# Optimization experiments

Measured on AMD Instinct MI355X. Metric: run time of the kernel, lower is better.

## Reference

```python
import jax, jax.numpy as jnp
import numpy as np

N, D, H, L = 100000, 128, 4, 2
C = D // H  # per-head channels
E = 1600000
NEG_SLOPE = 0.2
LN_EPS = 1e-5


def setup_inputs() -> dict:
    key = jax.random.key(0)
    ks = jax.random.split(key, 8)
    x = jax.random.normal(ks[0], (N, D), dtype=jnp.float32)
    edge_index = jax.random.randint(ks[1], (2, E), 0, N, dtype=jnp.int64)
    s = 1.0 / np.sqrt(D)
    Wl = jax.random.normal(ks[2], (L, D, D), dtype=jnp.float32) * s
    Wr = jax.random.normal(ks[3], (L, D, D), dtype=jnp.float32) * s
    att = jax.random.normal(ks[4], (L, H, C), dtype=jnp.float32) * (1.0 / np.sqrt(C))
    bias = jnp.zeros((L, D), dtype=jnp.float32)
    gamma = jnp.ones((L, D), dtype=jnp.float32)
    beta = jnp.zeros((L, D), dtype=jnp.float32)
    return {"x": x, "edge_index": edge_index, "Wl": Wl, "Wr": Wr,
            "att": att, "bias": bias, "gamma": gamma, "beta": beta}


def _gatv2_layer(h, src, dst, Wl, Wr, att, bias):
    # h: (N, D); src/dst: (E2,) with self-loops already appended
    xl = (h @ Wl).reshape(N, H, C)  # source-side transform
    xr = (h @ Wr).reshape(N, H, C)  # target-side transform
    e = jax.nn.leaky_relu(xl[src] + xr[dst], NEG_SLOPE)      # (E2, H, C)
    alpha = jnp.einsum('ehc,hc->eh', e, att)                 # (E2, H)
    # segment softmax over incoming edges of each destination node
    m = jax.ops.segment_max(alpha, dst, num_segments=N)      # (N, H)
    ea = jnp.exp(alpha - m[dst])
    s = jax.ops.segment_sum(ea, dst, num_segments=N)         # (N, H)
    a = ea / s[dst]                                          # (E2, H)
    out = jax.ops.segment_sum(a[:, :, None] * xl[src], dst, num_segments=N)
    return out.reshape(N, D) + bias


def _layer_norm(y, gamma, beta):
    mu = jnp.mean(y, axis=-1, keepdims=True)
    var = jnp.var(y, axis=-1, keepdims=True)
    return (y - mu) * jax.lax.rsqrt(var + LN_EPS) * gamma + beta


def reference(x, edge_index, Wl, Wr, att, bias, gamma, beta):
    # PyG GATv2Conv defaults: add_self_loops=True (eval mode: dropouts identity)
    loops = jnp.arange(N, dtype=edge_index.dtype)
    src = jnp.concatenate([edge_index[0], loops])
    dst = jnp.concatenate([edge_index[1], loops])
    h = x
    for l in range(L):
        g = _gatv2_layer(h, src, dst, Wl[l], Wr[l], att[l], bias[l])
        h = h + jax.nn.elu(_layer_norm(g, gamma[l], beta[l]))
    return h
```

## Files before the change

kernel.cpp:

```cpp
#include <hip/hip_runtime.h>
#include <hip/hip_fp16.h>
#include <math.h>

#define N_NODES 100000
#define D_FEAT  128
#define E_EDGES 1600000
#define E2      (E_EDGES + N_NODES)
#define NEG_SLOPE 0.2f
#define LN_EPS    1e-5f

#define NB   391
#define TS   8192
#define NTIL ((E2 + TS - 1) / TS)

typedef __attribute__((ext_vector_type(8))) short short8;
typedef __attribute__((ext_vector_type(4))) float floatx4;
typedef _Float16 h2 __attribute__((ext_vector_type(2)));

static __device__ __forceinline__ float fdot2f(h2 a, h2 b, float c) {
#if __has_builtin(__builtin_amdgcn_fdot2)
    return __builtin_amdgcn_fdot2(a, b, c, false);
#else
    return (float)a[0] * (float)b[0] + (float)a[1] * (float)b[1] + c;
#endif
}

__global__ __launch_bounds__(256) void bucket_count(const int* __restrict__ edge_dst,
                                                    int* __restrict__ bcnt) {
    __shared__ int h[NB];
    const int t = threadIdx.x;
    for (int i = t; i < NB; i += 256) h[i] = 0;
    __syncthreads();
    const int base = blockIdx.x * TS;
#pragma unroll
    for (int j = 0; j < TS / 256; ++j) {
        int i = base + j * 256 + t;
        if (i < E2) {
            int d = (i < E_EDGES) ? edge_dst[i] : (i - E_EDGES);
            atomicAdd(&h[d >> 8], 1);
        }
    }
    __syncthreads();
    for (int i = t; i < NB; i += 256)
        if (h[i]) atomicAdd(&bcnt[i], h[i]);
}

__global__ __launch_bounds__(512) void bucket_scan(const int* __restrict__ bcnt,
                                                   int* __restrict__ bstart,
                                                   int* __restrict__ bcur,
                                                   int* __restrict__ rowstart) {
    __shared__ int s[512];
    const int t = threadIdx.x;
    s[t] = (t < NB) ? bcnt[t] : 0;
    __syncthreads();
    for (int off = 1; off < 512; off <<= 1) {
        int x = (t >= off) ? s[t - off] : 0;
        __syncthreads();
        s[t] += x;
        __syncthreads();
    }
    int excl = (t == 0) ? 0 : s[t - 1];
    if (t < NB) { bstart[t] = excl; bcur[t] = excl; }
    if (t == NB) bstart[NB] = excl;
    if (t == 0) rowstart[N_NODES] = E2;
}

__global__ __launch_bounds__(256) void bucket_scatter(const int* __restrict__ edge_src,
                                                      const int* __restrict__ edge_dst,
                                                      int* __restrict__ bcur,
                                                      uint2* __restrict__ pairbuf) {
    __shared__ int h[NB];
    __shared__ int cur[NB];
    const int t = threadIdx.x;
    for (int i = t; i < NB; i += 256) h[i] = 0;
    __syncthreads();
    const int base = blockIdx.x * TS;
#pragma unroll
    for (int j = 0; j < TS / 256; ++j) {
        int i = base + j * 256 + t;
        if (i < E2) {
            int d = (i < E_EDGES) ? edge_dst[i] : (i - E_EDGES);
            atomicAdd(&h[d >> 8], 1);
        }
    }
    __syncthreads();
    for (int i = t; i < NB; i += 256)
        cur[i] = h[i] ? atomicAdd(&bcur[i], h[i]) : 0;
    __syncthreads();
#pragma unroll
    for (int j = 0; j < TS / 256; ++j) {
        int i = base + j * 256 + t;
        if (i < E2) {
            int d, sr;
            if (i < E_EDGES) { d = edge_dst[i]; sr = edge_src[i]; }
            else             { d = i - E_EDGES; sr = d; }
            int pos = atomicAdd(&cur[d >> 8], 1);
            pairbuf[pos] = (uint2){(unsigned)sr, (unsigned)d};
        }
    }
}

__global__ __launch_bounds__(256) void bucketize(const uint2* __restrict__ pairbuf,
                                                 const int* __restrict__ bstart,
                                                 int* __restrict__ rowstart,
                                                 int* __restrict__ csr_src) {
    __shared__ int cnt[256], sc[256], cur[256];
    const int blk = blockIdx.x;
    const int t = threadIdx.x;
    const int nbase = blk << 8;
    cnt[t] = 0;
    __syncthreads();
    const int e0 = bstart[blk], e1 = bstart[blk + 1];
    for (int p = e0 + t; p < e1; p += 256) {
        uint2 pr = pairbuf[p];
        atomicAdd(&cnt[pr.y - nbase], 1);
    }
    __syncthreads();
    sc[t] = cnt[t];
    __syncthreads();
    for (int off = 1; off < 256; off <<= 1) {
        int x = (t >= off) ? sc[t - off] : 0;
        __syncthreads();
        sc[t] += x;
        __syncthreads();
    }
    int excl = (t == 0) ? 0 : sc[t - 1];
    int node = nbase + t;
    if (node < N_NODES) rowstart[node] = e0 + excl;
    cur[t] = e0 + excl;
    __syncthreads();
    for (int p = e0 + t; p < e1; p += 256) {
        uint2 pr = pairbuf[p];
        int pos = atomicAdd(&cur[pr.y - nbase], 1);
        csr_src[pos] = (int)pr.x;
    }
}

static __device__ __forceinline__ unsigned short f2bf(float f) {
    unsigned u = __float_as_uint(f);
    unsigned r = (u + 0x7fffu + ((u >> 16) & 1u)) >> 16;
    return (unsigned short)r;
}

__global__ void cvt_bf16(const float* __restrict__ in,
                         unsigned short* __restrict__ out, int n4) {
    int i = blockIdx.x * blockDim.x + threadIdx.x;
    if (i >= n4) return;
    float4 v = ((const float4*)in)[i];
    ushort4 o;
    o.x = f2bf(v.x); o.y = f2bf(v.y); o.z = f2bf(v.z); o.w = f2bf(v.w);
    ((ushort4*)out)[i] = o;
}

__global__ void prep_wt(const float* __restrict__ Wl, const float* __restrict__ Wr,
                        const float* __restrict__ att,
                        unsigned short* __restrict__ Wt, _Float16* __restrict__ atth) {
    int idx = blockIdx.x * 256 + threadIdx.x;
    if (idx < 65536) {
        int l    = idx >> 15;
        int rem  = idx & 32767;
        int side = rem >> 14;
        int cw   = rem & 16383;
        int col  = cw >> 7, k = cw & 127;
        const float* W = side ? Wr : Wl;
        Wt[idx] = f2bf(W[l * 16384 + k * 128 + col]);
    } else if (idx < 65536 + 256) {
        int j = idx - 65536;
        atth[j] = (_Float16)att[j];
    }
}

__global__ __launch_bounds__(256) void gemm_mfma2(
        const unsigned short* __restrict__ hbf,
        const unsigned short* __restrict__ Wt,
        _Float16* __restrict__ xl, _Float16* __restrict__ xr, int n_rows) {
    const int wave = threadIdx.x >> 6;
    const int lane = threadIdx.x & 63;
    const int m = lane & 15;
    const int q = lane >> 4;
    const int r0 = (blockIdx.x * 4 + wave) * 32;

    int arow0 = r0 + m;        if (arow0 >= n_rows) arow0 = n_rows - 1;
    int arow1 = r0 + 16 + m;   if (arow1 >= n_rows) arow1 = n_rows - 1;

    floatx4 acc[2][2][8];
#pragma unroll
    for (int s = 0; s < 2; ++s)
#pragma unroll
        for (int rt = 0; rt < 2; ++rt)
#pragma unroll
            for (int ct = 0; ct < 8; ++ct) acc[s][rt][ct] = (floatx4){0.f,0.f,0.f,0.f};

#pragma unroll
    for (int ks = 0; ks < 4; ++ks) {
        const int k0 = ks * 32 + q * 8;
        short8 a0 = *(const short8*)(hbf + (size_t)arow0 * 128 + k0);
        short8 a1 = *(const short8*)(hbf + (size_t)arow1 * 128 + k0);
#pragma unroll
        for (int s = 0; s < 2; ++s) {
#pragma unroll
            for (int ct = 0; ct < 8; ++ct) {
                short8 b = *(const short8*)(Wt + (size_t)s * 16384
                                            + (size_t)(ct * 16 + m) * 128 + k0);
                acc[s][0][ct] = __builtin_amdgcn_mfma_f32_16x16x32_bf16(a0, b, acc[s][0][ct], 0, 0, 0);
                acc[s][1][ct] = __builtin_amdgcn_mfma_f32_16x16x32_bf16(a1, b, acc[s][1][ct], 0, 0, 0);
            }
        }
    }

#pragma unroll
    for (int s = 0; s < 2; ++s) {
        _Float16* out = s ? xr : xl;
#pragma unroll
        for (int rt = 0; rt < 2; ++rt)
#pragma unroll
            for (int ct = 0; ct < 8; ++ct)
#pragma unroll
                for (int i = 0; i < 4; ++i) {
                    int row = r0 + rt * 16 + q * 4 + i;
                    if (row < n_rows)
                        out[(size_t)row * 128 + ct * 16 + m] = (_Float16)acc[s][rt][ct][i];
                }
    }
}

union U16 { uint4 u; h2 h[4]; };

__global__ __launch_bounds__(256) void gat_node5(
        const _Float16* __restrict__ xl,
        const _Float16* __restrict__ xr,
        const float* __restrict__ h_in,
        const int* __restrict__ rowstart, const int* __restrict__ csr_src,
        const _Float16* __restrict__ atth, const float* __restrict__ bias,
        const float* __restrict__ gamma, const float* __restrict__ beta,
        float* __restrict__ h_out, unsigned* __restrict__ hbf_out) {
    __shared__ float lacc[4][8 * 136];
    __shared__ float lS[4][4];

    const int wave = threadIdx.x >> 6;
    const int lane = threadIdx.x & 63;
    const int node = blockIdx.x * 4 + wave;
    const int esub = lane >> 3;
    const int r    = lane & 7;
    const int c0   = r * 16;

    U16 xra, xrb, ata, atb;
    {
        const uint4* xp = (const uint4*)(xr + (size_t)node * 128 + c0);
        xra.u = xp[0]; xrb.u = xp[1];
        const uint4* ap = (const uint4*)(atth + c0);
        ata.u = ap[0]; atb.u = ap[1];
    }
    const h2 ns2 = {(_Float16)NEG_SLOPE, (_Float16)NEG_SLOPE};

    const int p0 = rowstart[node], p1 = rowstart[node + 1];
    float s = 0.f;
    h2 acc2[8];
#pragma unroll
    for (int j = 0; j < 8; ++j) acc2[j] = (h2){(_Float16)0.f, (_Float16)0.f};

    const unsigned short* xls = (const unsigned short*)xl;

    int pb = p0;
    bool v = (pb + esub) < p1;
    U16 a0, a1;
    {
        int pc = v ? (pb + esub) : (p1 - 1);
        int src = csr_src[pc];
        const uint4* rp = (const uint4*)(xls + (size_t)src * 128 + c0);
        a0.u = rp[0]; a1.u = rp[1];
    }

    while (pb < p1) {
        const int pbn = pb + 8;
        U16 b0, b1;
        bool vn = false;
        if (pbn < p1) {
            vn = (pbn + esub) < p1;
            int pcn = vn ? (pbn + esub) : (p1 - 1);
            int srcn = csr_src[pcn];
            const uint4* rpn = (const uint4*)(xls + (size_t)srcn * 128 + c0);
            b0.u = rpn[0]; b1.u = rpn[1];
        }

        float d = 0.f;
#pragma unroll
        for (int qq = 0; qq < 4; ++qq) {
            h2 z  = a0.h[qq] + xra.h[qq];
            h2 lk = __builtin_elementwise_max(z, z * ns2);
            d = fdot2f(lk, ata.h[qq], d);
        }
#pragma unroll
        for (int qq = 0; qq < 4; ++qq) {
            h2 z  = a1.h[qq] + xrb.h[qq];
            h2 lk = __builtin_elementwise_max(z, z * ns2);
            d = fdot2f(lk, atb.h[qq], d);
        }
        float alpha = d + __shfl_xor(d, 1);
        float w = v ? __expf(alpha) : 0.f;
        s += w;
        h2 w2 = {(_Float16)w, (_Float16)w};
#pragma unroll
        for (int qq = 0; qq < 4; ++qq)
            acc2[qq] = w2 * a0.h[qq] + acc2[qq];
#pragma unroll
        for (int qq = 0; qq < 4; ++qq)
            acc2[qq + 4] = w2 * a1.h[qq] + acc2[qq + 4];

        a0 = b0; a1 = b1; v = vn; pb = pbn;
    }

    float ssum = s;
    ssum += __shfl_xor(ssum, 8);
    ssum += __shfl_xor(ssum, 16);
    ssum += __shfl_xor(ssum, 32);

    float* lb = &lacc[wave][esub * 136 + c0];
#pragma unroll
    for (int qq = 0; qq < 4; ++qq) {
        h2 lo = acc2[2 * qq], hi = acc2[2 * qq + 1];
        float4 o = {(float)lo[0], (float)lo[1], (float)hi[0], (float)hi[1]};
        *(float4*)(lb + 4 * qq) = o;
    }
    if (esub == 0 && (r & 1) == 0) lS[wave][r >> 1] = ssum;
    __syncthreads();

    const int c = lane * 2;
    float S = lS[wave][lane >> 4];
    float g0 = 0.f, g1 = 0.f;
#pragma unroll
    for (int e = 0; e < 8; ++e) {
        float2 f = *(const float2*)(&lacc[wave][e * 136 + c]);
        g0 += f.x; g1 += f.y;
    }
    const float invS = 1.f / S;
    g0 = g0 * invS + bias[c];
    g1 = g1 * invS + bias[c + 1];

    float sum = g0 + g1, sq = g0 * g0 + g1 * g1;
#pragma unroll
    for (int off = 1; off < 64; off <<= 1) {
        sum += __shfl_xor(sum, off);
        sq  += __shfl_xor(sq, off);
    }
    float mu   = sum * (1.f / 128.f);
    float var  = sq * (1.f / 128.f) - mu * mu;
    float rstd = rsqrtf(var + LN_EPS);
    float y0 = (g0 - mu) * rstd * gamma[c]     + beta[c];
    float y1 = (g1 - mu) * rstd * gamma[c + 1] + beta[c + 1];
    float e0 = (y0 > 0.f) ? y0 : (__expf(y0) - 1.f);
    float e1 = (y1 > 0.f) ? y1 : (__expf(y1) - 1.f);

    const float2 hv = *(const float2*)(h_in + (size_t)node * 128 + c);
    float2 o;
    o.x = hv.x + e0;
    o.y = hv.y + e1;
    *(float2*)(h_out + (size_t)node * 128 + c) = o;
    if (hbf_out) {
        unsigned pk = (unsigned)f2bf(o.x) | ((unsigned)f2bf(o.y) << 16);
        hbf_out[(size_t)node * 64 + lane] = pk;
    }
}

extern "C" void kernel_launch(void* const* d_in, const int* in_sizes, int n_in,
                              void* d_out, int out_size, void* d_ws, size_t ws_size,
                              hipStream_t stream) {
    const float* x     = (const float*)d_in[0];
    const int*   eidx  = (const int*)d_in[1];
    const float* Wl    = (const float*)d_in[2];
    const float* Wr    = (const float*)d_in[3];
    const float* att   = (const float*)d_in[4];
    const float* bias  = (const float*)d_in[5];
    const float* gamma = (const float*)d_in[6];
    const float* beta  = (const float*)d_in[7];
    float* out = (float*)d_out;

    char* ws = (char*)d_ws;
    _Float16* xl = (_Float16*)ws;              ws += (size_t)N_NODES * 128 * 2;
    _Float16* xr = (_Float16*)ws;              ws += (size_t)N_NODES * 128 * 2;
    float* h1 = (float*)ws;                    ws += (size_t)N_NODES * 128 * 4;
    unsigned short* hbf = (unsigned short*)ws; ws += (size_t)N_NODES * 128 * 2;
    unsigned short* Wt  = (unsigned short*)ws; ws += (size_t)65536 * 2;
    _Float16* atth = (_Float16*)ws;            ws += 256 * 2;
    uint2* pairbuf = (uint2*)ws;               ws += (size_t)E2 * 8;
    int* bcnt     = (int*)ws; ws += (NB + 1) * 4;
    int* bstart   = (int*)ws; ws += (NB + 1) * 4;
    int* bcur     = (int*)ws; ws += (NB + 1) * 4;
    int* rowstart = (int*)ws; ws += (size_t)(N_NODES + 4) * 4;
    int* csr_src  = (int*)ws; ws += (size_t)E2 * 4;

    const int* edge_src = eidx;
    const int* edge_dst = eidx + E_EDGES;

    const int n4 = N_NODES * 128 / 4;
    cvt_bf16<<<(n4 + 255) / 256, 256, 0, stream>>>(x, hbf, n4);
    prep_wt<<<257, 256, 0, stream>>>(Wl, Wr, att, Wt, atth);

    (void)hipMemsetAsync(bcnt, 0, (NB + 1) * 4, stream);
    bucket_count<<<NTIL, 256, 0, stream>>>(edge_dst, bcnt);
    bucket_scan<<<1, 512, 0, stream>>>(bcnt, bstart, bcur, rowstart);
    bucket_scatter<<<NTIL, 256, 0, stream>>>(edge_src, edge_dst, bcur, pairbuf);
    bucketize<<<NB, 256, 0, stream>>>(pairbuf, bstart, rowstart, csr_src);

    const int gemm_gx = (N_NODES + 127) / 128;
    for (int l = 0; l < 2; ++l) {
        const float* hin  = (l == 0) ? x  : h1;
        float*       hout = (l == 1) ? out : h1;
        gemm_mfma2<<<gemm_gx, 256, 0, stream>>>(
            hbf, Wt + (size_t)l * 32768, xl, xr, N_NODES);
        gat_node5<<<N_NODES / 4, 256, 0, stream>>>(
            xl, xr, hin, rowstart, csr_src,
            atth + l * 128, bias + l * 128, gamma + l * 128, beta + l * 128,
            hout, (l == 0) ? (unsigned*)hbf : nullptr);
    }
}
```

Measured before the change: 429.3 us.

## Rework CSR build, fuse bf16 cast into GEMM, deepen gather prefetch

Measured after the change: 400.1 us. -6.8%, faster.

```diff
diff --git a/kernel.cpp b/kernel.cpp
--- a/kernel.cpp
+++ b/kernel.cpp
@@ -25,33 +25,51 @@
 #endif
 }
 
-__global__ __launch_bounds__(256) void bucket_count(const int* __restrict__ edge_dst,
-                                                    int* __restrict__ bcnt) {
+__global__ __launch_bounds__(1024) void tile_count(const int* __restrict__ edge_dst,
+                                                   int* __restrict__ tcnt) {
     __shared__ int h[NB];
     const int t = threadIdx.x;
-    for (int i = t; i < NB; i += 256) h[i] = 0;
+    if (t < NB) h[t] = 0;
     __syncthreads();
     const int base = blockIdx.x * TS;
 #pragma unroll
-    for (int j = 0; j < TS / 256; ++j) {
-        int i = base + j * 256 + t;
+    for (int j = 0; j < TS / 1024; ++j) {
+        int i = base + j * 1024 + t;
         if (i < E2) {
             int d = (i < E_EDGES) ? edge_dst[i] : (i - E_EDGES);
             atomicAdd(&h[d >> 8], 1);
         }
     }
     __syncthreads();
-    for (int i = t; i < NB; i += 256)
-        if (h[i]) atomicAdd(&bcnt[i], h[i]);
+    if (t < NB) tcnt[blockIdx.x * NB + t] = h[t];
+}
+
+__global__ __launch_bounds__(256) void col_scan(const int* __restrict__ tcnt,
+                                                int* __restrict__ toff,
+                                                int* __restrict__ bcnt) {
+    __shared__ int s[256];
+    const int b = blockIdx.x;
+    const int t = threadIdx.x;
+    int v = (t < NTIL) ? tcnt[t * NB + b] : 0;
+    s[t] = v;
+    __syncthreads();
+    for (int off = 1; off < 256; off <<= 1) {
+        int x = (t >= off) ? s[t - off] : 0;
+        __syncthreads();
+        s[t] += x;
+        __syncthreads();
+    }
+    if (t < NTIL) toff[t * NB + b] = s[t] - v;
+    if (t == 255) bcnt[b] = s[255];
 }
 
 __global__ __launch_bounds__(512) void bucket_scan(const int* __restrict__ bcnt,
                                                    int* __restrict__ bstart,
-                                                   int* __restrict__ bcur,
                                                    int* __restrict__ rowstart) {
     __shared__ int s[512];
     const int t = threadIdx.x;
-    s[t] = (t < NB) ? bcnt[t] : 0;
+    int v = (t < NB) ? bcnt[t] : 0;
+    s[t] = v;
     __syncthreads();
     for (int off = 1; off < 512; off <<= 1) {
         int x = (t >= off) ? s[t - off] : 0;
@@ -59,80 +77,69 @@
         s[t] += x;
         __syncthreads();
     }
-    int excl = (t == 0) ? 0 : s[t - 1];
-    if (t < NB) { bstart[t] = excl; bcur[t] = excl; }
-    if (t == NB) bstart[NB] = excl;
+    if (t <= NB) bstart[t] = s[t] - v;
     if (t == 0) rowstart[N_NODES] = E2;
 }
 
-__global__ __launch_bounds__(256) void bucket_scatter(const int* __restrict__ edge_src,
-                                                      const int* __restrict__ edge_dst,
-                                                      int* __restrict__ bcur,
-                                                      uint2* __restrict__ pairbuf) {
-    __shared__ int h[NB];
+__global__ __launch_bounds__(1024) void tile_scatter(const int* __restrict__ edge_src,
+                                                     const int* __restrict__ edge_dst,
+                                                     const int* __restrict__ bstart,
+                                                     const int* __restrict__ toff,
+                                                     unsigned* __restrict__ pairbuf) {
+    __shared__ int base[NB];
     __shared__ int cur[NB];
     const int t = threadIdx.x;
-    for (int i = t; i < NB; i += 256) h[i] = 0;
-    __syncthreads();
-    const int base = blockIdx.x * TS;
-#pragma unroll
-    for (int j = 0; j < TS / 256; ++j) {
-        int i = base + j * 256 + t;
-        if (i < E2) {
-            int d = (i < E_EDGES) ? edge_dst[i] : (i - E_EDGES);
-            atomicAdd(&h[d >> 8], 1);
-        }
-    }
-    __syncthreads();
-    for (int i = t; i < NB; i += 256)
-        cur[i] = h[i] ? atomicAdd(&bcur[i], h[i]) : 0;
-    __syncthreads();
-#pragma unroll
-    for (int j = 0; j < TS / 256; ++j) {
-        int i = base + j * 256 + t;
+    if (t < NB) { base[t] = bstart[t] + toff[blockIdx.x * NB + t]; cur[t] = 0; }
+    __syncthreads();
+    const int tb = blockIdx.x * TS;
+#pragma unroll
+    for (int j = 0; j < TS / 1024; ++j) {
+        int i = tb + j * 1024 + t;
         if (i < E2) {
             int d, sr;
             if (i < E_EDGES) { d = edge_dst[i]; sr = edge_src[i]; }
             else             { d = i - E_EDGES; sr = d; }
-            int pos = atomicAdd(&cur[d >> 8], 1);
-            pairbuf[pos] = (uint2){(unsigned)sr, (unsigned)d};
-        }
-    }
-}
-
-__global__ __launch_bounds__(256) void bucketize(const uint2* __restrict__ pairbuf,
-                                                 const int* __restrict__ bstart,
-                                                 int* __restrict__ rowstart,
-                                                 int* __restrict__ csr_src) {
+            int b = d >> 8;
+            int rank = atomicAdd(&cur[b], 1);
+            pairbuf[base[b] + rank] = (unsigned)sr | ((unsigned)(d & 255) << 17);
+        }
+    }
+}
+
+__global__ __launch_bounds__(1024) void bucketize(const unsigned* __restrict__ pairbuf,
+                                                  const int* __restrict__ bstart,
+                                                  int* __restrict__ rowstart,
+                                                  int* __restrict__ csr_src) {
     __shared__ int cnt[256], sc[256], cur[256];
     const int blk = blockIdx.x;
     const int t = threadIdx.x;
     const int nbase = blk << 8;
-    cnt[t] = 0;
+    if (t < 256) cnt[t] = 0;
     __syncthreads();
     const int e0 = bstart[blk], e1 = bstart[blk + 1];
-    for (int p = e0 + t; p < e1; p += 256) {
-        uint2 pr = pairbuf[p];
-        atomicAdd(&cnt[pr.y - nbase], 1);
-    }
-    __syncthreads();
-    sc[t] = cnt[t];
+    for (int p = e0 + t; p < e1; p += 1024)
+        atomicAdd(&cnt[pairbuf[p] >> 17], 1);
+    __syncthreads();
+    int v = (t < 256) ? cnt[t] : 0;
+    if (t < 256) sc[t] = v;
     __syncthreads();
     for (int off = 1; off < 256; off <<= 1) {
-        int x = (t >= off) ? sc[t - off] : 0;
-        __syncthreads();
-        sc[t] += x;
-        __syncthreads();
-    }
-    int excl = (t == 0) ? 0 : sc[t - 1];
-    int node = nbase + t;
-    if (node < N_NODES) rowstart[node] = e0 + excl;
-    cur[t] = e0 + excl;
-    __syncthreads();
-    for (int p = e0 + t; p < e1; p += 256) {
-        uint2 pr = pairbuf[p];
-        int pos = atomicAdd(&cur[pr.y - nbase], 1);
-        csr_src[pos] = (int)pr.x;
+        int x = (t < 256 && t >= off) ? sc[t - off] : 0;
+        __syncthreads();
+        if (t < 256) sc[t] += x;
+        __syncthreads();
+    }
+    if (t < 256) {
+        int excl = sc[t] - v;
+        int node = nbase + t;
+        if (node < N_NODES) rowstart[node] = e0 + excl;
+        cur[t] = e0 + excl;
+    }
+    __syncthreads();
+    for (int p = e0 + t; p < e1; p += 1024) {
+        unsigned pr = pairbuf[p];
+        int pos = atomicAdd(&cur[pr >> 17], 1);
+        csr_src[pos] = (int)(pr & 0x1FFFF);
     }
 }
 
@@ -140,16 +147,6 @@
     unsigned u = __float_as_uint(f);
     unsigned r = (u + 0x7fffu + ((u >> 16) & 1u)) >> 16;
     return (unsigned short)r;
-}
-
-__global__ void cvt_bf16(const float* __restrict__ in,
-                         unsigned short* __restrict__ out, int n4) {
-    int i = blockIdx.x * blockDim.x + threadIdx.x;
-    if (i >= n4) return;
-    float4 v = ((const float4*)in)[i];
-    ushort4 o;
-    o.x = f2bf(v.x); o.y = f2bf(v.y); o.z = f2bf(v.z); o.w = f2bf(v.w);
-    ((ushort4*)out)[i] = o;
 }
 
 __global__ void prep_wt(const float* __restrict__ Wl, const float* __restrict__ Wr,
@@ -172,6 +169,7 @@
 
 __global__ __launch_bounds__(256) void gemm_mfma2(
         const unsigned short* __restrict__ hbf,
+        const float* __restrict__ Afp,
         const unsigned short* __restrict__ Wt,
         _Float16* __restrict__ xl, _Float16* __restrict__ xr, int n_rows) {
     const int wave = threadIdx.x >> 6;
@@ -194,8 +192,20 @@
 #pragma unroll
     for (int ks = 0; ks < 4; ++ks) {
         const int k0 = ks * 32 + q * 8;
-        short8 a0 = *(const short8*)(hbf + (size_t)arow0 * 128 + k0);
-        short8 a1 = *(const short8*)(hbf + (size_t)arow1 * 128 + k0);
+        short8 a0, a1;
+        if (Afp) {
+            float4 f0 = *(const float4*)(Afp + (size_t)arow0 * 128 + k0);
+            float4 f1 = *(const float4*)(Afp + (size_t)arow0 * 128 + k0 + 4);
+            float4 g0 = *(const float4*)(Afp + (size_t)arow1 * 128 + k0);
+            float4 g1 = *(const float4*)(Afp + (size_t)arow1 * 128 + k0 + 4);
+            a0 = (short8){(short)f2bf(f0.x), (short)f2bf(f0.y), (short)f2bf(f0.z), (short)f2bf(f0.w),
+                          (short)f2bf(f1.x), (short)f2bf(f1.y), (short)f2bf(f1.z), (short)f2bf(f1.w)};
+            a1 = (short8){(short)f2bf(g0.x), (short)f2bf(g0.y), (short)f2bf(g0.z), (short)f2bf(g0.w),
+                          (short)f2bf(g1.x), (short)f2bf(g1.y), (short)f2bf(g1.z), (short)f2bf(g1.w)};
+        } else {
+            a0 = *(const short8*)(hbf + (size_t)arow0 * 128 + k0);
+            a1 = *(const short8*)(hbf + (size_t)arow1 * 128 + k0);
+        }
 #pragma unroll
         for (int s = 0; s < 2; ++s) {
 #pragma unroll
@@ -226,7 +236,7 @@
 
 union U16 { uint4 u; h2 h[4]; };
 
-__global__ __launch_bounds__(256) void gat_node5(
+__global__ __launch_bounds__(256) void gat_node6(
         const _Float16* __restrict__ xl,
         const _Float16* __restrict__ xr,
         const float* __restrict__ h_in,
@@ -262,25 +272,32 @@
     const unsigned short* xls = (const unsigned short*)xl;
 
     int pb = p0;
-    bool v = (pb + esub) < p1;
-    U16 a0, a1;
+    bool vA = (p0 + esub) < p1;
+    U16 a0, a1, b0, b1;
     {
-        int pc = v ? (pb + esub) : (p1 - 1);
+        int pc = vA ? (p0 + esub) : (p1 - 1);
         int src = csr_src[pc];
         const uint4* rp = (const uint4*)(xls + (size_t)src * 128 + c0);
         a0.u = rp[0]; a1.u = rp[1];
     }
+    bool vB = false;
+    if (p0 + 8 < p1) {
+        vB = (p0 + 8 + esub) < p1;
+        int pc = vB ? (p0 + 8 + esub) : (p1 - 1);
+        int src = csr_src[pc];
+        const uint4* rp = (const uint4*)(xls + (size_t)src * 128 + c0);
+        b0.u = rp[0]; b1.u = rp[1];
+    }
 
     while (pb < p1) {
-        const int pbn = pb + 8;
-        U16 b0, b1;
-        bool vn = false;
-        if (pbn < p1) {
-            vn = (pbn + esub) < p1;
-            int pcn = vn ? (pbn + esub) : (p1 - 1);
-            int srcn = csr_src[pcn];
-            const uint4* rpn = (const uint4*)(xls + (size_t)srcn * 128 + c0);
-            b0.u = rpn[0]; b1.u = rpn[1];
+        U16 c0v, c1v;
+        bool vC = false;
+        if (pb + 16 < p1) {
+            vC = (pb + 16 + esub) < p1;
+            int pc = vC ? (pb + 16 + esub) : (p1 - 1);
+            int src = csr_src[pc];
+            const uint4* rp = (const uint4*)(xls + (size_t)src * 128 + c0);
+            c0v.u = rp[0]; c1v.u = rp[1];
         }
 
         float d = 0.f;
@@ -297,7 +314,7 @@
             d = fdot2f(lk, atb.h[qq], d);
         }
         float alpha = d + __shfl_xor(d, 1);
-        float w = v ? __expf(alpha) : 0.f;
+        float w = vA ? __expf(alpha) : 0.f;
         s += w;
         h2 w2 = {(_Float16)w, (_Float16)w};
 #pragma unroll
@@ -307,7 +324,9 @@
         for (int qq = 0; qq < 4; ++qq)
             acc2[qq + 4] = w2 * a1.h[qq] + acc2[qq + 4];
 
-        a0 = b0; a1 = b1; v = vn; pb = pbn;
+        a0 = b0; a1 = b1; vA = vB;
+        b0 = c0v; b1 = c1v; vB = vC;
+        pb += 8;
     }
 
     float ssum = s;
@@ -323,7 +342,6 @@
         *(float4*)(lb + 4 * qq) = o;
     }
     if (esub == 0 && (r & 1) == 0) lS[wave][r >> 1] = ssum;
-    __syncthreads();
 
     const int c = lane * 2;
     float S = lS[wave][lane >> 4];
@@ -382,33 +400,32 @@
     unsigned short* hbf = (unsigned short*)ws; ws += (size_t)N_NODES * 128 * 2;
     unsigned short* Wt  = (unsigned short*)ws; ws += (size_t)65536 * 2;
     _Float16* atth = (_Float16*)ws;            ws += 256 * 2;
-    uint2* pairbuf = (uint2*)ws;               ws += (size_t)E2 * 8;
+    unsigned* pairbuf = (unsigned*)ws;         ws += (size_t)E2 * 4;
+    int* tcnt     = (int*)ws; ws += (size_t)NTIL * NB * 4;
+    int* toff     = (int*)ws; ws += (size_t)NTIL * NB * 4;
     int* bcnt     = (int*)ws; ws += (NB + 1) * 4;
     int* bstart   = (int*)ws; ws += (NB + 1) * 4;
-    int* bcur     = (int*)ws; ws += (NB + 1) * 4;
     int* rowstart = (int*)ws; ws += (size_t)(N_NODES + 4) * 4;
     int* csr_src  = (int*)ws; ws += (size_t)E2 * 4;
 
     const int* edge_src = eidx;
     const int* edge_dst = eidx + E_EDGES;
 
-    const int n4 = N_NODES * 128 / 4;
-    cvt_bf16<<<(n4 + 255) / 256, 256, 0, stream>>>(x, hbf, n4);
     prep_wt<<<257, 256, 0, stream>>>(Wl, Wr, att, Wt, atth);
 
-    (void)hipMemsetAsync(bcnt, 0, (NB + 1) * 4, stream);
-    bucket_count<<<NTIL, 256, 0, stream>>>(edge_dst, bcnt);
-    bucket_scan<<<1, 512, 0, stream>>>(bcnt, bstart, bcur, rowstart);
-    bucket_scatter<<<NTIL, 256, 0, stream>>>(edge_src, edge_dst, bcur, pairbuf);
-    bucketize<<<NB, 256, 0, stream>>>(pairbuf, bstart, rowstart, csr_src);
+    tile_count<<<NTIL, 1024, 0, stream>>>(edge_dst, tcnt);
+    col_scan<<<NB, 256, 0, stream>>>(tcnt, toff, bcnt);
+    bucket_scan<<<1, 512, 0, stream>>>(bcnt, bstart, rowstart);
+    tile_scatter<<<NTIL, 1024, 0, stream>>>(edge_src, edge_dst, bstart, toff, pairbuf);
+    bucketize<<<NB, 1024, 0, stream>>>(pairbuf, bstart, rowstart, csr_src);
 
     const int gemm_gx = (N_NODES + 127) / 128;
     for (int l = 0; l < 2; ++l) {
         const float* hin  = (l == 0) ? x  : h1;
         float*       hout = (l == 1) ? out : h1;
         gemm_mfma2<<<gemm_gx, 256, 0, stream>>>(
-            hbf, Wt + (size_t)l * 32768, xl, xr, N_NODES);
-        gat_node5<<<N_NODES / 4, 256, 0, stream>>>(
+            hbf, (l == 0) ? x : nullptr, Wt + (size_t)l * 32768, xl, xr, N_NODES);
+        gat_node6<<<N_NODES / 4, 256, 0, stream>>>(
             xl, xr, hin, rowstart, csr_src,
             atth + l * 128, bias + l * 128, gamma + l * 128, beta + l * 128,
             hout, (l == 0) ? (unsigned*)hbf : nullptr);
```
